# Kernel optimization log

Measured on AMD Instinct MI355X. Metric: run time of the kernel, lower is better.

## Reference

```python
import jax, jax.numpy as jnp
import numpy as np

B, N, C, H = 64, 1024, 512, 8
D = C // H            # head dim = 64
WIN = 32
M = 64                # num_landmarks
HP, WP = 8, 8         # closest_square_factors(64)
ITERS = 6
SCALE = D ** -0.5


def activ(x):
    # ExpLinearAfterThreshold with max_val=0: exp(clamp(x, max=0)) + relu(x)
    return jnp.exp(jnp.minimum(x, 0.0)) + jax.nn.relu(x)


def moore_penrose_iter_pinv(x, iters=ITERS):
    abs_x = jnp.abs(x)
    denom = jnp.max(abs_x.sum(axis=-1)) * jnp.max(abs_x.sum(axis=-2))
    z = jnp.swapaxes(x, -1, -2) / denom
    I = jnp.eye(x.shape[-1], dtype=x.dtype)
    for _ in range(iters):
        xz = x @ z
        z = 0.25 * z @ (13.0 * I - xz @ (15.0 * I - xz @ (7.0 * I - xz)))
    return z


def pool_landmarks(t):
    t = t.reshape(B, H, HP, WIN // HP, WP, WIN // WP, D)
    return t.mean(axis=(3, 5)).reshape(B, H, M, D)


def setup_inputs() -> dict:
    key = jax.random.key(0)
    ks = jax.random.split(key, 7)
    s = 0.02
    x = jax.random.normal(ks[0], (B, N, C), jnp.float32)
    Wq = jax.random.normal(ks[1], (C, C), jnp.float32) * s
    bq = jnp.zeros((C,), jnp.float32)
    Wkv = jax.random.normal(ks[2], (C, 2 * C), jnp.float32) * s
    bkv = jnp.zeros((2 * C,), jnp.float32)
    Wp = jax.random.normal(ks[3], (C, C), jnp.float32) * s
    bp = jnp.zeros((C,), jnp.float32)
    return {"x": x, "Wq": Wq, "bq": bq, "Wkv": Wkv, "bkv": bkv, "Wp": Wp, "bp": bp}


def reference(x, Wq, bq, Wkv, bkv, Wp, bp):
    Bsz = x.shape[0]
    q = (x @ Wq + bq).reshape(Bsz, N, H, D).transpose(0, 2, 1, 3) * SCALE  # [B,H,N,D]
    kv = (x @ Wkv + bkv).reshape(Bsz, N, 2, H, D).transpose(2, 0, 3, 1, 4)
    k, v = kv[0], kv[1]                                                    # [B,H,N,D]

    q_m = pool_landmarks(q)   # [B,H,M,D]
    k_m = pool_landmarks(k)   # [B,H,M,D]

    temp = activ(jnp.einsum('bhmd,bhnd->bhmn', q_m, k_m))   # [B,H,M,M]
    pinv = moore_penrose_iter_pinv(temp, ITERS)

    v1 = jnp.concatenate([v, jnp.ones_like(v[..., :1])], axis=-1)          # [B,H,N,D+1]
    kern_qkm = activ(jnp.einsum('bhnd,bhmd->bhnm', q, k_m))                # [B,H,N,M]
    kern_qmk_v = activ(jnp.einsum('bhmd,bhnd->bhmn', q_m, k)) @ v1         # [B,H,M,D+1]

    prod = kern_qkm @ (pinv @ kern_qmk_v)                                  # [B,H,N,D+1]
    out = prod[..., :-1] / (prod[..., -1:] + 1e-12)                        # [B,H,N,D]
    out = out.transpose(0, 2, 1, 3).reshape(Bsz, N, C)
    return out @ Wp + bp
```

## Files before the change

### kernel.cpp

```cpp
#include <hip/hip_runtime.h>

typedef _Float16 f16;
typedef _Float16 f16x4 __attribute__((ext_vector_type(4)));
typedef _Float16 f16x8 __attribute__((ext_vector_type(8)));
typedef float f32x4 __attribute__((ext_vector_type(4)));

#define MFMA16(a, b, c) __builtin_amdgcn_mfma_f32_16x16x32_f16((a), (b), (c), 0, 0, 0)

__device__ __forceinline__ void gload16(const void* g, void* l) {
  __builtin_amdgcn_global_load_lds(
      (const __attribute__((address_space(1))) void*)g,
      (__attribute__((address_space(3))) void*)l, 16, 0, 0);
}

__device__ __forceinline__ f16x8 lds8(const f16* buf, int row, int ch) {
  return *(const f16x8*)(buf + row * 64 + ((ch ^ (row & 7)) << 3));
}

#define VMW8 asm volatile("s_waitcnt vmcnt(8)" ::: "memory")
#define VMW0 asm volatile("s_waitcnt vmcnt(0)" ::: "memory")
#define BAR __builtin_amdgcn_s_barrier()


__global__ __launch_bounds__(256) void k_prep(
    const float* __restrict__ x, const float* __restrict__ Wq,
    const float* __restrict__ Wkv, const float* __restrict__ Wp,
    const float* __restrict__ bq, const float* __restrict__ bkv,
    f16* __restrict__ xh, float* __restrict__ xm, f16* __restrict__ WcT,
    f16* __restrict__ WpT, float* __restrict__ bc,
    unsigned* __restrict__ den) {
  __shared__ float pl[4][8][512];
  int bid = blockIdx.x;
  int tid = threadIdx.x;
  if (bid >= 512) {
    int b = bid - 512;
    if (b < 1536) {
      for (int kk = tid; kk < 512; kk += 256) {
        float w = (b < 512) ? Wq[kk * 512 + b] : Wkv[kk * 1024 + (b - 512)];
        WcT[b * 512 + kk] = (f16)w;
      }
      if (tid == 0) bc[b] = (b < 512) ? bq[b] : bkv[b - 512];
      if (b == 0 && tid == 1) { den[0] = 0u; den[1] = 0u; }
    } else {
      int pc = b - 1536;
      for (int kk = tid; kk < 512; kk += 256)
        WpT[pc * 512 + kk] = (f16)Wp[kk * 512 + pc];
    }
    return;
  }
  int b = bid >> 3, a = bid & 7;
  int tr = tid >> 6, cl = tid & 63;
  int c0 = cl * 8;
  float pacc[8][8];
#pragma unroll
  for (int i = 0; i < 8; i++)
#pragma unroll
    for (int j = 0; j < 8; j++) pacc[i][j] = 0.f;
#pragma unroll
  for (int j = 0; j < 32; j++) {
    int n = a * 128 + tr * 32 + j;
    const float* row = x + (size_t)(b * 1024 + n) * 512 + c0;
    float4 v0 = *(const float4*)row;
    float4 v1 = *(const float4*)(row + 4);
    f16x8 h;
    h[0] = (f16)v0.x; h[1] = (f16)v0.y; h[2] = (f16)v0.z; h[3] = (f16)v0.w;
    h[4] = (f16)v1.x; h[5] = (f16)v1.y; h[6] = (f16)v1.z; h[7] = (f16)v1.w;
    *(f16x8*)(xh + (size_t)(b * 1024 + n) * 512 + c0) = h;
    int cg = j >> 2;
    pacc[cg][0] += v0.x; pacc[cg][1] += v0.y; pacc[cg][2] += v0.z;
    pacc[cg][3] += v0.w; pacc[cg][4] += v1.x; pacc[cg][5] += v1.y;
    pacc[cg][6] += v1.z; pacc[cg][7] += v1.w;
  }
#pragma unroll
  for (int cg = 0; cg < 8; cg++) {
    *(float4*)&pl[tr][cg][c0] =
        make_float4(pacc[cg][0], pacc[cg][1], pacc[cg][2], pacc[cg][3]);
    *(float4*)&pl[tr][cg][c0 + 4] =
        make_float4(pacc[cg][4], pacc[cg][5], pacc[cg][6], pacc[cg][7]);
  }
  __syncthreads();
#pragma unroll
  for (int s = 0; s < 4; s++) {
    int o = tid + s * 256;
    int cg = o >> 7, c4 = (o & 127) << 2;
    float4 r0 = *(const float4*)&pl[0][cg][c4];
    float4 r1 = *(const float4*)&pl[1][cg][c4];
    float4 r2 = *(const float4*)&pl[2][cg][c4];
    float4 r3 = *(const float4*)&pl[3][cg][c4];
    float4 r;
    r.x = (r0.x + r1.x + r2.x + r3.x) * 0.0625f;
    r.y = (r0.y + r1.y + r2.y + r3.y) * 0.0625f;
    r.z = (r0.z + r1.z + r2.z + r3.z) * 0.0625f;
    r.w = (r0.w + r1.w + r2.w + r3.w) * 0.0625f;
    *(float4*)(xm + (size_t)(b * 64 + a * 8 + cg) * 512 + c4) = r;
  }
}

__global__ __launch_bounds__(512) void k_qkv(
    const f16* __restrict__ xh, const f16* __restrict__ WcT,
    const float* __restrict__ bc, f16* __restrict__ qb, f16* __restrict__ kb,
    f16* __restrict__ vb) {
  __shared__ f16 Al[2][256 * 64];
  __shared__ f16 Bl[2][256 * 64];
  int bid = blockIdx.x;
  int swz = (bid & 7) * 192 + (bid >> 3);
  int ct = swz % 6, rt = swz / 6;
  int m0 = rt * 256, n0 = ct * 256;
  int tid = threadIdx.x, lane = tid & 63, w = tid >> 6;
  int lr = lane & 15, hi = lane >> 4;
  int wr = w >> 2, wc = w & 3;

  int srow = tid >> 3;
  int cg = (tid & 7) ^ (srow & 7);
  const f16* gA = xh + (size_t)(m0 + srow) * 512 + cg * 8;
  const f16* gB = WcT + (size_t)(n0 + srow) * 512 + cg * 8;

  f32x4 acc[4][8] = {};

#define STG(BUF, K0)                                                \
  {                                                                 \
    _Pragma("unroll") for (int s = 0; s < 4; s++) {                 \
      gload16(gA + (K0) + s * 64 * 512, &Al[BUF][tid * 8 + s * 4096]); \
      gload16(gB + (K0) + s * 64 * 512, &Bl[BUF][tid * 8 + s * 4096]); \
    }                                                               \
  }
#define CMP(BUF)                                                    \
  {                                                                 \
    __builtin_amdgcn_s_setprio(1);                                  \
    _Pragma("unroll") for (int kc = 0; kc < 2; kc++) {              \
      f16x8 af[4], bf[8];                                           \
      _Pragma("unroll") for (int ni = 0; ni < 4; ni++)              \
          af[ni] = lds8(&Bl[BUF][0], wc * 64 + ni * 16 + lr, kc * 4 + hi); \
      _Pragma("unroll") for (int mi = 0; mi < 8; mi++)              \
          bf[mi] = lds8(&Al[BUF][0], wr * 128 + mi * 16 + lr, kc * 4 + hi); \
      _Pragma("unroll") for (int ni = 0; ni < 4; ni++)              \
          _Pragma("unroll") for (int mi = 0; mi < 8; mi++)          \
              acc[ni][mi] = MFMA16(af[ni], bf[mi], acc[ni][mi]);    \
    }                                                               \
    __builtin_amdgcn_s_setprio(0);                                  \
  }

  STG(0, 0);
  STG(1, 64);
  VMW8; BAR; CMP(0); BAR; STG(0, 2 * 64);
  VMW8; BAR; CMP(1); BAR; STG(1, 3 * 64);
  VMW8; BAR; CMP(0); BAR; STG(0, 4 * 64);
  VMW8; BAR; CMP(1); BAR; STG(1, 5 * 64);
  VMW8; BAR; CMP(0); BAR; STG(0, 6 * 64);
  VMW8; BAR; CMP(1); BAR; STG(1, 7 * 64);
  VMW8; BAR; CMP(0);
  VMW0; BAR; CMP(1);
#undef STG
#undef CMP

  int region = n0 >> 9;
  f16* dst = region == 0 ? qb : (region == 1 ? kb : vb);
  float scale = region == 0 ? 0.125f : 1.0f;
  int ncol0 = n0 - region * 512;
  float4 bias[4];
#pragma unroll
  for (int ni = 0; ni < 4; ni++)
    bias[ni] = *(const float4*)(bc + region * 512 + ncol0 + wc * 64 + ni * 16 +
                                hi * 4);
#pragma unroll
  for (int mi = 0; mi < 8; mi++) {
    int gr = m0 + wr * 128 + mi * 16 + lr;
    int b = gr >> 10, n = gr & 1023;
#pragma unroll
    for (int ni = 0; ni < 4; ni++) {
      int cc = ncol0 + wc * 64 + ni * 16 + hi * 4;
      int h = cc >> 6, d = cc & 63;
      f16x4 hv;
      hv[0] = (f16)((acc[ni][mi][0] + bias[ni].x) * scale);
      hv[1] = (f16)((acc[ni][mi][1] + bias[ni].y) * scale);
      hv[2] = (f16)((acc[ni][mi][2] + bias[ni].z) * scale);
      hv[3] = (f16)((acc[ni][mi][3] + bias[ni].w) * scale);
      *(f16x4*)(dst + (size_t)(((b * 8 + h) * 1024 + n) * 64 + d)) = hv;
    }
  }
}

__global__ __launch_bounds__(512) void k_qmkm(
    const float* __restrict__ xm, const float* __restrict__ Wq,
    const float* __restrict__ Wkv, const float* __restrict__ bq,
    const float* __restrict__ bkv, float* __restrict__ qm,
    float* __restrict__ km) {
  __shared__ float xl[16][512];
  int bid = blockIdx.x;
  int b = bid >> 2, mg = bid & 3;
  int tid = threadIdx.x;
  for (int s = 0; s < 4; s++) {
    int idx = (tid + s * 512) * 4;
    int r = idx >> 9, cc = idx & 511;
    *(float4*)&xl[r][cc] =
        *(const float4*)(xm + (b * 64 + mg * 16 + r) * 512 + cc);
  }
  __syncthreads();
  int oc = tid;
  float aq[16] = {}, ak[16] = {};
  for (int cc = 0; cc < 512; cc += 4) {
    float wq0 = Wq[(cc + 0) * 512 + oc], wq1 = Wq[(cc + 1) * 512 + oc];
    float wq2 = Wq[(cc + 2) * 512 + oc], wq3 = Wq[(cc + 3) * 512 + oc];
    float wk0 = Wkv[(cc + 0) * 1024 + oc], wk1 = Wkv[(cc + 1) * 1024 + oc];
    float wk2 = Wkv[(cc + 2) * 1024 + oc], wk3 = Wkv[(cc + 3) * 1024 + oc];
    for (int mi = 0; mi < 16; mi++) {
      float4 xv = *(const float4*)&xl[mi][cc];
      aq[mi] += xv.x * wq0 + xv.y * wq1 + xv.z * wq2 + xv.w * wq3;
      ak[mi] += xv.x * wk0 + xv.y * wk1 + xv.z * wk2 + xv.w * wk3;
    }
  }
  int h = oc >> 6, d = oc & 63;
  for (int mi = 0; mi < 16; mi++) {
    int m = mg * 16 + mi;
    int base = ((b * 8 + h) * 64 + m) * 64 + d;
    qm[base] = (aq[mi] + bq[oc]) * 0.125f;
    km[base] = ak[mi] + bkv[oc];
  }
}

__global__ __launch_bounds__(256) void k_temp(const float* __restrict__ qm,
                                              const float* __restrict__ km,
                                              float* __restrict__ temp,
                                              unsigned* __restrict__ den) {
  __shared__ float ql[64][68], kl[64][68];
  __shared__ float rs[64], cs[64];
  int g = blockIdx.x, tid = threadIdx.x;
  for (int idx = tid; idx < 4096; idx += 256) {
    int r = idx >> 6, c = idx & 63;
    ql[r][c] = qm[g * 4096 + idx];
    kl[r][c] = km[g * 4096 + idx];
  }
  __syncthreads();
  int ti = tid >> 4, tj = tid & 15;
  float acc[4][4] = {};
  for (int kk = 0; kk < 64; kk += 4) {
    float4 qa[4], kb[4];
    for (int i = 0; i < 4; i++) qa[i] = *(const float4*)&ql[ti * 4 + i][kk];
    for (int j = 0; j < 4; j++) kb[j] = *(const float4*)&kl[tj * 4 + j][kk];
    for (int i = 0; i < 4; i++)
      for (int j = 0; j < 4; j++)
        acc[i][j] += qa[i].x * kb[j].x + qa[i].y * kb[j].y +
                     qa[i].z * kb[j].z + qa[i].w * kb[j].w;
  }
  float e[4][4];
  for (int i = 0; i < 4; i++)
    for (int j = 0; j < 4; j++) {
      float xx = acc[i][j];
      e[i][j] = xx > 0.f ? 1.f + xx : __expf(xx);
    }
  __syncthreads();
  for (int i = 0; i < 4; i++)
    for (int j = 0; j < 4; j++) kl[ti * 4 + i][tj * 4 + j] = e[i][j];
  __syncthreads();
  for (int idx = tid; idx < 4096; idx += 256)
    temp[g * 4096 + idx] = kl[idx >> 6][idx & 63];
  if (tid < 64) {
    float s = 0.f;
    for (int j = 0; j < 64; j++) s += kl[tid][j];
    rs[tid] = s;
  } else if (tid < 128) {
    int c = tid - 64;
    float s = 0.f;
    for (int i = 0; i < 64; i++) s += kl[i][c];
    cs[c] = s;
  }
  __syncthreads();
  if (tid == 0) {
    float mx = rs[0];
    for (int i = 1; i < 64; i++) mx = fmaxf(mx, rs[i]);
    atomicMax(den + 0, __float_as_uint(mx));
  }
  if (tid == 1) {
    float mx = cs[0];
    for (int i = 1; i < 64; i++) mx = fmaxf(mx, cs[i]);
    atomicMax(den + 1, __float_as_uint(mx));
  }
}

__global__ __launch_bounds__(256) void k_pinv(const float* __restrict__ temp,
                                              const unsigned* __restrict__ den,
                                              float* __restrict__ z) {
  __shared__ f16 wh[64][72], Zh[64][72], ZhT[64][72], GhT[64][72], W1h[64][72],
      W2h[64][72];
  __shared__ float colZ[64];
  int g = blockIdx.x, tid = threadIdx.x;
  float dn = __uint_as_float(den[0]) * __uint_as_float(den[1]);
  float inv = 1.0f / dn;
  for (int idx = tid; idx < 4096; idx += 256) {
    int r = idx >> 6, c = idx & 63;
    float t = temp[g * 4096 + idx];
    wh[r][c] = (f16)(t - 1.0f);
    ZhT[r][c] = (f16)(t * inv);
  }
  __syncthreads();
  for (int idx = tid; idx < 4096; idx += 256) {
    int r = idx >> 6, c = idx & 63;
    Zh[r][c] = ZhT[c][r];
  }
  __syncthreads();
  int lane = tid & 63, w = tid >> 6, lr = lane & 15, hi = lane >> 4;
  int rb = w * 16;
  for (int it = 0; it < 6; it++) {
    if (tid < 64) {
      float s = 0.f;
      for (int i = 0; i < 64; i++) s += (float)ZhT[tid][i];
      colZ[tid] = s;
    }
    __syncthreads();
    {
      f32x4 acc[4] = {};
      for (int kc = 0; kc < 2; kc++) {
        f16x8 a = *(const f16x8*)&wh[rb + lr][kc * 32 + hi * 8];
        for (int cj = 0; cj < 4; cj++)
          acc[cj] = MFMA16(
              a, *(const f16x8*)&ZhT[cj * 16 + lr][kc * 32 + hi * 8], acc[cj]);
      }
      for (int cj = 0; cj < 4; cj++)
        for (int rg = 0; rg < 4; rg++) {
          int rr = rb + hi * 4 + rg, cc = cj * 16 + lr;
          GhT[cc][rr] = (f16)(acc[cj][rg] + colZ[cc]);
        }
    }
    __syncthreads();
    {
      f32x4 acc[4] = {};
      for (int kc = 0; kc < 2; kc++) {
        f16x8 a = *(const f16x8*)&Zh[rb + lr][kc * 32 + hi * 8];
        for (int cj = 0; cj < 4; cj++)
          acc[cj] = MFMA16(
              a, *(const f16x8*)&GhT[cj * 16 + lr][kc * 32 + hi * 8], acc[cj]);
      }
      for (int cj = 0; cj < 4; cj++)
        for (int rg = 0; rg < 4; rg++)
          W1h[rb + hi * 4 + rg][cj * 16 + lr] = (f16)acc[cj][rg];
    }
    __syncthreads();
    {
      f32x4 acc[4] = {};
      for (int kc = 0; kc < 2; kc++) {
        f16x8 a = *(const f16x8*)&W1h[rb + lr][kc * 32 + hi * 8];
        for (int cj = 0; cj < 4; cj++)
          acc[cj] = MFMA16(
              a, *(const f16x8*)&GhT[cj * 16 + lr][kc * 32 + hi * 8], acc[cj]);
      }
      for (int cj = 0; cj < 4; cj++)
        for (int rg = 0; rg < 4; rg++)
          W2h[rb + hi * 4 + rg][cj * 16 + lr] = (f16)acc[cj][rg];
    }
    __syncthreads();
    {
      f32x4 acc[4] = {};
      for (int kc = 0; kc < 2; kc++) {
        f16x8 a = *(const f16x8*)&W2h[rb + lr][kc * 32 + hi * 8];
        for (int cj = 0; cj < 4; cj++)
          acc[cj] = MFMA16(
              a, *(const f16x8*)&GhT[cj * 16 + lr][kc * 32 + hi * 8], acc[cj]);
      }
      for (int cj = 0; cj < 4; cj++)
        for (int rg = 0; rg < 4; rg++) {
          int rr = rb + hi * 4 + rg, cc = cj * 16 + lr;
          float zn = 3.25f * (float)Zh[rr][cc] - 3.75f * (float)W1h[rr][cc] +
                     1.75f * (float)W2h[rr][cc] - 0.25f * acc[cj][rg];
          if (it == 5) {
            z[g * 4096 + rr * 64 + cc] = zn;
          } else {
            Zh[rr][cc] = (f16)zn;
            ZhT[cc][rr] = (f16)zn;
          }
        }
    }
    __syncthreads();
  }
}

__global__ __launch_bounds__(256) void k_kwa(
    const float* __restrict__ qm, const f16* __restrict__ kb,
    const f16* __restrict__ vb, const float* __restrict__ zz,
    const float* __restrict__ km, const f16* __restrict__ qb,
    f16* __restrict__ attn) {
  __shared__ __align__(16) char smem[76288];
  int g = blockIdx.x, tid = threadIdx.x;
  int lane = tid & 63, w = tid >> 6, lr = lane & 15, hi = lane >> 4;
  int srow8 = tid >> 3;
  int cgs = (tid & 7) ^ (srow8 & 7);
  f16* klp = (f16*)(smem + 59904);
  f16(*qh)[72] = (f16(*)[72])smem;
  f16(*vt)[136] = (f16(*)[136])(smem + 9216);
  f16(*Slk)[136] = (f16(*)[136])(smem + 30976);
  f16(*w2l)[72] = (f16(*)[72])(smem + 48384);
  for (int idx = tid; idx < 4096; idx += 256) {
    int r = idx >> 6, c = idx & 63;
    qh[r][c] = (f16)qm[g * 4096 + idx];
  }
  for (int idx = tid; idx < 16 * 136; idx += 256) {
    int r = 64 + idx / 136, c = idx % 136;
    vt[r][c] = (r == 64) ? (f16)1.0f : (f16)0.0f;
  }
  f32x4 acc2[5] = {};
  const f16* kbase = kb + (size_t)g * 65536;
  const f16* vbase = vb + (size_t)g * 65536;
  for (int n0 = 0; n0 < 1024; n0 += 128) {
    __syncthreads();
#pragma unroll
    for (int s = 0; s < 4; s++)
      gload16(kbase + (size_t)(n0 + srow8 + s * 32) * 64 + cgs * 8,
              klp + tid * 8 + s * 2048);
#pragma unroll
    for (int s = 0; s < 4; s++) {
      int cid = tid + s * 256;
      int r = cid >> 3, ch = cid & 7;
      f16x8 v8 = *(const f16x8*)(vbase + (size_t)(n0 + r) * 64 + ch * 8);
      for (int j = 0; j < 8; j++) vt[ch * 8 + j][r] = v8[j];
    }
    __syncthreads();
    f32x4 sacc[8] = {};
    for (int kc = 0; kc < 2; kc++) {
      f16x8 a = *(const f16x8*)&qh[w * 16 + lr][kc * 32 + hi * 8];
      for (int cj = 0; cj < 8; cj++)
        sacc[cj] = MFMA16(a, lds8(klp, cj * 16 + lr, kc * 4 + hi), sacc[cj]);
    }
    for (int cj = 0; cj < 8; cj++)
      for (int rg = 0; rg < 4; rg++) {
        float xx = sacc[cj][rg];
        Slk[w * 16 + hi * 4 + rg][cj * 16 + lr] =
            (f16)(xx > 0.f ? 1.f + xx : __expf(xx));
      }
    __syncthreads();
    for (int kc2 = 0; kc2 < 4; kc2++) {
      f16x8 a = *(const f16x8*)&Slk[w * 16 + lr][kc2 * 32 + hi * 8];
      for (int ce = 0; ce < 5; ce++)
        acc2[ce] = MFMA16(
            a, *(const f16x8*)&vt[ce * 16 + lr][kc2 * 32 + hi * 8], acc2[ce]);
    }
  }
  __syncthreads();
  float(*kql)[84] = (float(*)[84])smem;
  float(*zl)[68] = (float(*)[68])(smem + 30976);
  for (int ce = 0; ce < 5; ce++)
    for (int rg = 0; rg < 4; rg++)
      kql[w * 16 + hi * 4 + rg][ce * 16 + lr] = acc2[ce][rg];
  for (int idx = tid; idx < 4096; idx += 256)
    zl[idx >> 6][idx & 63] = zz[g * 4096 + idx];
  __syncthreads();
  {
    int ti = tid >> 4, tj = tid & 15;
    float acc[4][5] = {};
    for (int kk = 0; kk < 64; kk++) {
      float a0 = zl[ti * 4 + 0][kk], a1 = zl[ti * 4 + 1][kk];
      float a2 = zl[ti * 4 + 2][kk], a3 = zl[ti * 4 + 3][kk];
      for (int j = 0; j < 5; j++) {
        float bv = kql[kk][tj * 5 + j];
        acc[0][j] += a0 * bv; acc[1][j] += a1 * bv;
        acc[2][j] += a2 * bv; acc[3][j] += a3 * bv;
      }
    }
    for (int i = 0; i < 4; i++)
      for (int j = 0; j < 5; j++)
        w2l[tj * 5 + j][ti * 4 + i] = (f16)acc[i][j];
  }
  __syncthreads();
  f16(*kmh)[72] = (f16(*)[72])smem;
  f16(*Sl)[72] = (f16(*)[72])(smem + 9216);
  int b = g >> 3, h = g & 7;
  for (int idx = tid; idx < 4096; idx += 256)
    kmh[idx >> 6][idx & 63] = (f16)km[g * 4096 + idx];
  __syncthreads();
  const f16* qgb = qb + (size_t)g * 65536;
  for (int nt = 0; nt < 8; nt++) {
    int n0 = nt * 128;
    if (nt) __syncthreads();
#pragma unroll
    for (int s = 0; s < 4; s++)
      gload16(qgb + (size_t)(n0 + srow8 + s * 32) * 64 + cgs * 8,
              klp + tid * 8 + s * 2048);
    __syncthreads();
    f32x4 sacc[2][4] = {};
    for (int kc = 0; kc < 2; kc++)
      for (int ri = 0; ri < 2; ri++) {
        f16x8 a = lds8(klp, w * 32 + ri * 16 + lr, kc * 4 + hi);
        for (int cj = 0; cj < 4; cj++)
          sacc[ri][cj] = MFMA16(
              a, *(const f16x8*)&kmh[cj * 16 + lr][kc * 32 + hi * 8],
              sacc[ri][cj]);
      }
    for (int ri = 0; ri < 2; ri++)
      for (int cj = 0; cj < 4; cj++)
        for (int rg = 0; rg < 4; rg++) {
          float xx = sacc[ri][cj][rg];
          Sl[w * 32 + ri * 16 + hi * 4 + rg][cj * 16 + lr] =
              (f16)(xx > 0.f ? 1.f + xx : __expf(xx));
        }
    __syncthreads();
    f32x4 accP[5][2] = {};
    for (int kc = 0; kc < 2; kc++)
      for (int ri = 0; ri < 2; ri++) {
        f16x8 bfrag =
            *(const f16x8*)&Sl[w * 32 + ri * 16 + lr][kc * 32 + hi * 8];
        for (int ce = 0; ce < 5; ce++)
          accP[ce][ri] = MFMA16(
              *(const f16x8*)&w2l[ce * 16 + lr][kc * 32 + hi * 8], bfrag,
              accP[ce][ri]);
      }
    for (int ri = 0; ri < 2; ri++) {
      float dv = __shfl(accP[4][ri][0], lr, 64);
      float rd = 1.0f / (dv + 1e-12f);
      int n = w * 32 + ri * 16 + lr;
      for (int ce = 0; ce < 4; ce++) {
        f16x4 hv;
        hv[0] = (f16)(accP[ce][ri][0] * rd);
        hv[1] = (f16)(accP[ce][ri][1] * rd);
        hv[2] = (f16)(accP[ce][ri][2] * rd);
        hv[3] = (f16)(accP[ce][ri][3] * rd);
        *(f16x4*)(attn + (size_t)(b * 1024 + n0 + n) * 512 + h * 64 +
                  ce * 16 + hi * 4) = hv;
      }
    }
  }
}

__global__ __launch_bounds__(512) void k_out(const f16* __restrict__ ah,
                                             const f16* __restrict__ WpT,
                                             const float* __restrict__ bp,
                                             float* __restrict__ out) {
  __shared__ f16 Al[2][256 * 64];
  __shared__ f16 Bl[2][256 * 64];
  int bid = blockIdx.x;
  int swz = (bid & 7) * 64 + (bid >> 3);
  int ct = swz & 1, rt = swz >> 1;
  int m0 = rt * 256, n0 = ct * 256;
  int tid = threadIdx.x, lane = tid & 63, w = tid >> 6;
  int lr = lane & 15, hi = lane >> 4;
  int wr = w >> 2, wc = w & 3;

  int srow = tid >> 3;
  int cg = (tid & 7) ^ (srow & 7);
  const f16* gA = ah + (size_t)(m0 + srow) * 512 + cg * 8;
  const f16* gB = WpT + (size_t)(n0 + srow) * 512 + cg * 8;

  f32x4 acc[4][8] = {};

#define STG(BUF, K0)                                                \
  {                                                                 \
    _Pragma("unroll") for (int s = 0; s < 4; s++) {                 \
      gload16(gA + (K0) + s * 64 * 512, &Al[BUF][tid * 8 + s * 4096]); \
      gload16(gB + (K0) + s * 64 * 512, &Bl[BUF][tid * 8 + s * 4096]); \
    }                                                               \
  }
#define CMP(BUF)                                                    \
  {                                                                 \
    __builtin_amdgcn_s_setprio(1);                                  \
    _Pragma("unroll") for (int kc = 0; kc < 2; kc++) {              \
      f16x8 af[4], bf[8];                                           \
      _Pragma("unroll") for (int ni = 0; ni < 4; ni++)              \
          af[ni] = lds8(&Bl[BUF][0], wc * 64 + ni * 16 + lr, kc * 4 + hi); \
      _Pragma("unroll") for (int mi = 0; mi < 8; mi++)              \
          bf[mi] = lds8(&Al[BUF][0], wr * 128 + mi * 16 + lr, kc * 4 + hi); \
      _Pragma("unroll") for (int ni = 0; ni < 4; ni++)              \
          _Pragma("unroll") for (int mi = 0; mi < 8; mi++)          \
              acc[ni][mi] = MFMA16(af[ni], bf[mi], acc[ni][mi]);    \
    }                                                               \
    __builtin_amdgcn_s_setprio(0);                                  \
  }

  STG(0, 0);
  STG(1, 64);
  VMW8; BAR; CMP(0); BAR; STG(0, 2 * 64);
  VMW8; BAR; CMP(1); BAR; STG(1, 3 * 64);
  VMW8; BAR; CMP(0); BAR; STG(0, 4 * 64);
  VMW8; BAR; CMP(1); BAR; STG(1, 5 * 64);
  VMW8; BAR; CMP(0); BAR; STG(0, 6 * 64);
  VMW8; BAR; CMP(1); BAR; STG(1, 7 * 64);
  VMW8; BAR; CMP(0);
  VMW0; BAR; CMP(1);
#undef STG
#undef CMP

  float4 bias[4];
#pragma unroll
  for (int ni = 0; ni < 4; ni++)
    bias[ni] = *(const float4*)(bp + n0 + wc * 64 + ni * 16 + hi * 4);
#pragma unroll
  for (int mi = 0; mi < 8; mi++) {
    int gr = m0 + wr * 128 + mi * 16 + lr;
#pragma unroll
    for (int ni = 0; ni < 4; ni++) {
      int gc = n0 + wc * 64 + ni * 16 + hi * 4;
      float4 v;
      v.x = acc[ni][mi][0] + bias[ni].x;
      v.y = acc[ni][mi][1] + bias[ni].y;
      v.z = acc[ni][mi][2] + bias[ni].z;
      v.w = acc[ni][mi][3] + bias[ni].w;
      *(float4*)(out + (size_t)gr * 512 + gc) = v;
    }
  }
}

extern "C" void kernel_launch(void* const* d_in, const int* in_sizes, int n_in,
                              void* d_out, int out_size, void* d_ws,
                              size_t ws_size, hipStream_t stream) {
  (void)in_sizes; (void)n_in; (void)out_size; (void)ws_size;
  const float* x = (const float*)d_in[0];
  const float* Wq = (const float*)d_in[1];
  const float* bq = (const float*)d_in[2];
  const float* Wkv = (const float*)d_in[3];
  const float* bkv = (const float*)d_in[4];
  const float* Wp = (const float*)d_in[5];
  const float* bp = (const float*)d_in[6];
  float* outp = (float*)d_out;

  char* ws = (char*)d_ws;
  size_t o = 0;
  auto take = [&](size_t bytes) {
    char* p = ws + o;
    o += (bytes + 255) & ~(size_t)255;
    return p;
  };
  f16* WcT = (f16*)take(1536 * 512 * 2);
  f16* WpT = (f16*)take(512 * 512 * 2);
  float* bc = (float*)take(1536 * 4);
  f16* xh = (f16*)take(67108864);
  f16* qb = (f16*)take(67108864);
  f16* kb = (f16*)take(67108864);
  f16* vb = (f16*)take(67108864);

  char* od = (char*)d_out;
  size_t s = 0;
  auto sub = [&](size_t bytes) {
    char* p = od + s;
    s += (bytes + 255) & ~(size_t)255;
    return p;
  };
  float* xm = (float*)sub(64 * 64 * 512 * 4);
  float* qm = (float*)sub(512 * 4096 * 4);
  float* km = (float*)sub(512 * 4096 * 4);
  float* temp = (float*)sub(512 * 4096 * 4);
  float* zz = (float*)sub(512 * 4096 * 4);
  unsigned* den = (unsigned*)sub(256);
  f16* attn = xh;

  hipLaunchKernelGGL(k_prep, dim3(2560), dim3(256), 0, stream, x, Wq, Wkv, Wp,
                     bq, bkv, xh, xm, WcT, WpT, bc, den);
  hipLaunchKernelGGL(k_qkv, dim3(1536), dim3(512), 0, stream, xh, WcT, bc,
                     qb, kb, vb);
  hipLaunchKernelGGL(k_qmkm, dim3(256), dim3(512), 0, stream, xm, Wq, Wkv, bq,
                     bkv, qm, km);
  hipLaunchKernelGGL(k_temp, dim3(512), dim3(256), 0, stream, qm, km, temp,
                     den);
  hipLaunchKernelGGL(k_pinv, dim3(512), dim3(256), 0, stream, temp, den, zz);
  hipLaunchKernelGGL(k_kwa, dim3(512), dim3(256), 0, stream, qm, kb, vb, zz,
                     km, qb, attn);
  hipLaunchKernelGGL(k_out, dim3(512), dim3(512), 0, stream, attn, WpT, bp,
                     outp);
}
```

Before: 474.2 us.

## Prefetch next K/V and Q tiles during MFMA phases in attention kernel

Issues the global loads for the next 128-row K tile (LDS async) and V tile (into registers) right after the score computation, so they overlap the second MFMA phase. The Q-tile loads in the output loop get the same treatment, and the first Q tile is prefetched during the z·kq matmul. The single LDS buffer klp is reused, relying on barrier placement to avoid overwriting live data. In exchange it adds register pressure for the held V fragments and relies on implicit vmcnt waits at barriers.

```diff
diff --git a/kernel.cpp b/kernel.cpp
--- a/kernel.cpp
+++ b/kernel.cpp
@@ -399,19 +399,26 @@
   f32x4 acc2[5] = {};
   const f16* kbase = kb + (size_t)g * 65536;
   const f16* vbase = vb + (size_t)g * 65536;
+  int vrow = tid >> 3, vch = tid & 7;
+  f16x8 vr0, vr1, vr2, vr3;
+#pragma unroll
+  for (int s = 0; s < 4; s++)
+    gload16(kbase + (size_t)(srow8 + s * 32) * 64 + cgs * 8,
+            klp + tid * 8 + s * 2048);
+  vr0 = *(const f16x8*)(vbase + (size_t)vrow * 64 + vch * 8);
+  vr1 = *(const f16x8*)(vbase + (size_t)(vrow + 32) * 64 + vch * 8);
+  vr2 = *(const f16x8*)(vbase + (size_t)(vrow + 64) * 64 + vch * 8);
+  vr3 = *(const f16x8*)(vbase + (size_t)(vrow + 96) * 64 + vch * 8);
   for (int n0 = 0; n0 < 1024; n0 += 128) {
     __syncthreads();
 #pragma unroll
-    for (int s = 0; s < 4; s++)
-      gload16(kbase + (size_t)(n0 + srow8 + s * 32) * 64 + cgs * 8,
-              klp + tid * 8 + s * 2048);
-#pragma unroll
-    for (int s = 0; s < 4; s++) {
-      int cid = tid + s * 256;
-      int r = cid >> 3, ch = cid & 7;
-      f16x8 v8 = *(const f16x8*)(vbase + (size_t)(n0 + r) * 64 + ch * 8);
-      for (int j = 0; j < 8; j++) vt[ch * 8 + j][r] = v8[j];
-    }
+    for (int j = 0; j < 8; j++) vt[vch * 8 + j][vrow] = vr0[j];
+#pragma unroll
+    for (int j = 0; j < 8; j++) vt[vch * 8 + j][vrow + 32] = vr1[j];
+#pragma unroll
+    for (int j = 0; j < 8; j++) vt[vch * 8 + j][vrow + 64] = vr2[j];
+#pragma unroll
+    for (int j = 0; j < 8; j++) vt[vch * 8 + j][vrow + 96] = vr3[j];
     __syncthreads();
     f32x4 sacc[8] = {};
     for (int kc = 0; kc < 2; kc++) {
@@ -426,6 +433,17 @@
             (f16)(xx > 0.f ? 1.f + xx : __expf(xx));
       }
     __syncthreads();
+    if (n0 < 896) {
+      int nn = n0 + 128;
+#pragma unroll
+      for (int s = 0; s < 4; s++)
+        gload16(kbase + (size_t)(nn + srow8 + s * 32) * 64 + cgs * 8,
+                klp + tid * 8 + s * 2048);
+      vr0 = *(const f16x8*)(vbase + (size_t)(nn + vrow) * 64 + vch * 8);
+      vr1 = *(const f16x8*)(vbase + (size_t)(nn + vrow + 32) * 64 + vch * 8);
+      vr2 = *(const f16x8*)(vbase + (size_t)(nn + vrow + 64) * 64 + vch * 8);
+      vr3 = *(const f16x8*)(vbase + (size_t)(nn + vrow + 96) * 64 + vch * 8);
+    }
     for (int kc2 = 0; kc2 < 4; kc2++) {
       f16x8 a = *(const f16x8*)&Slk[w * 16 + lr][kc2 * 32 + hi * 8];
       for (int ce = 0; ce < 5; ce++)
@@ -442,6 +460,11 @@
   for (int idx = tid; idx < 4096; idx += 256)
     zl[idx >> 6][idx & 63] = zz[g * 4096 + idx];
   __syncthreads();
+  const f16* qgb = qb + (size_t)g * 65536;
+#pragma unroll
+  for (int s = 0; s < 4; s++)
+    gload16(qgb + (size_t)(srow8 + s * 32) * 64 + cgs * 8,
+            klp + tid * 8 + s * 2048);
   {
     int ti = tid >> 4, tj = tid & 15;
     float acc[4][5] = {};
@@ -465,15 +488,8 @@
   for (int idx = tid; idx < 4096; idx += 256)
     kmh[idx >> 6][idx & 63] = (f16)km[g * 4096 + idx];
   __syncthreads();
-  const f16* qgb = qb + (size_t)g * 65536;
   for (int nt = 0; nt < 8; nt++) {
     int n0 = nt * 128;
-    if (nt) __syncthreads();
-#pragma unroll
-    for (int s = 0; s < 4; s++)
-      gload16(qgb + (size_t)(n0 + srow8 + s * 32) * 64 + cgs * 8,
-              klp + tid * 8 + s * 2048);
-    __syncthreads();
     f32x4 sacc[2][4] = {};
     for (int kc = 0; kc < 2; kc++)
       for (int ri = 0; ri < 2; ri++) {
@@ -491,6 +507,12 @@
               (f16)(xx > 0.f ? 1.f + xx : __expf(xx));
         }
     __syncthreads();
+    if (nt < 7) {
+#pragma unroll
+      for (int s = 0; s < 4; s++)
+        gload16(qgb + (size_t)(n0 + 128 + srow8 + s * 32) * 64 + cgs * 8,
+                klp + tid * 8 + s * 2048);
+    }
     f32x4 accP[5][2] = {};
     for (int kc = 0; kc < 2; kc++)
       for (int ri = 0; ri < 2; ri++) {
@@ -515,6 +537,7 @@
                   ce * 16 + hi * 4) = hv;
       }
     }
+    __syncthreads();
   }
 }
 
```

New measurement: 473.9 us (median of 2 runs). No clear change (-0.1%).
